# Kernel optimization log

Hardware: AMD Instinct MI355X
Metric: run time of the kernel (lower is better)

## Reference

```python
import jax, jax.numpy as jnp
import numpy as np

T, B, H, L2, C = 1132, 128, 13, 100, 10  # seq, batch, hidden, total layers (2x50), classes


def setup_inputs() -> dict:
    key = jax.random.key(0)
    ks = jax.random.split(key, 7)
    s = 1.0 / np.sqrt(H)  # torch LSTM/Linear default init scale
    return {
        "input": jax.random.normal(ks[0], (B, T, H), jnp.float32),
        "w_ih": jax.random.uniform(ks[1], (L2, 4 * H, H), jnp.float32, -s, s),
        "w_hh": jax.random.uniform(ks[2], (L2, 4 * H, H), jnp.float32, -s, s),
        "b_ih": jax.random.uniform(ks[3], (L2, 4 * H), jnp.float32, -s, s),
        "b_hh": jax.random.uniform(ks[4], (L2, 4 * H), jnp.float32, -s, s),
        "w_lin": jax.random.uniform(ks[5], (C, T * H), jnp.float32, -1.0 / np.sqrt(T * H), 1.0 / np.sqrt(T * H)),
        "b_lin": jax.random.uniform(ks[6], (C,), jnp.float32, -1.0 / np.sqrt(T * H), 1.0 / np.sqrt(T * H)),
    }


def _lstm_stack(x, w_ih, w_hh, b_ih, b_hh):
    # x: [T, B, H]; weights stacked over layers: [L, 4H, H], biases [L, 4H]
    def layer(x, params):
        Wih, Whh, bih, bhh = params
        # input contribution for all timesteps at once (one big GEMM)
        pre = jnp.einsum('tbf,gf->tbg', x, Wih) + bih + bhh  # [T, B, 4H]

        def step(carry, p):
            h, c = carry
            g = p + h @ Whh.T  # [B, 4H]
            i, f, gg, o = jnp.split(g, 4, axis=-1)  # torch gate order: i,f,g,o
            c = jax.nn.sigmoid(f) * c + jax.nn.sigmoid(i) * jnp.tanh(gg)
            h = jax.nn.sigmoid(o) * jnp.tanh(c)
            return (h, c), h

        h0 = jnp.zeros((x.shape[1], Whh.shape[1]), x.dtype)
        _, hs = jax.lax.scan(step, (h0, h0), pre)
        return hs, None

    x, _ = jax.lax.scan(layer, x, (w_ih, w_hh, b_ih, b_hh))
    return x


def reference(input, w_ih, w_hh, b_ih, b_hh, w_lin, b_lin):
    x = jnp.transpose(input, (1, 0, 2))  # [T, B, H] (time-major for scan)
    x = _lstm_stack(x, w_ih, w_hh, b_ih, b_hh)
    x = jnp.transpose(x, (1, 0, 2)).reshape(input.shape[0], -1)  # [B, T*H]
    logits = x @ w_lin.T + b_lin
    return jax.nn.softmax(logits, axis=1)
```

## Files before the change

kernel.cpp:

```cpp
#include <hip/hip_runtime.h>
#include <stdint.h>

#define T_SEQ  1132
#define BATCH  128
#define HID    13
#define G4     52
#define NLAYER 100
#define NPIPE  8
#define LPW    4
#define NWGP   25
#define NTHR   384
#define CH     4
#define NCH    283
#define RCL    4
#define RC     8
#define NCLS   10
#define FEAT   (T_SEQ*HID)
#define L2E    1.44269504f

#define CHUNK_U32 (CH*256)
#define FLAG_BYTES 65536
#define RING_U32_PER_WG ((size_t)RC * CHUNK_U32)
#define RING_BYTES ((size_t)(NPIPE*NWGP) * RING_U32_PER_WG * 4)

typedef float  f32x4 __attribute__((ext_vector_type(4)));
typedef __fp16 f16x4 __attribute__((ext_vector_type(4)));
typedef unsigned int u32x4 __attribute__((ext_vector_type(4)));
typedef unsigned long long u64x2 __attribute__((ext_vector_type(2)));

struct HL { f16x4 h; f16x4 l; };

__device__ __forceinline__ void f16split(float x, __fp16& hi, __fp16& lo) {
  hi = (__fp16)x;
  lo = (__fp16)(x - (float)hi);
}

__device__ __forceinline__ void lspin_ge(int* p, int need) {
  int v = __hip_atomic_load(p, __ATOMIC_ACQUIRE, __HIP_MEMORY_SCOPE_WORKGROUP);
  while (v < need) {
    __builtin_amdgcn_s_sleep(1);
    v = __hip_atomic_load(p, __ATOMIC_ACQUIRE, __HIP_MEMORY_SCOPE_WORKGROUP);
  }
}
__device__ __forceinline__ void gspin_ge(int* p, int need) {
  int v = __hip_atomic_load(p, __ATOMIC_RELAXED, __HIP_MEMORY_SCOPE_AGENT);
  while (v < need) {
    __builtin_amdgcn_s_sleep(1);
    v = __hip_atomic_load(p, __ATOMIC_RELAXED, __HIP_MEMORY_SCOPE_AGENT);
  }
}

__global__ __launch_bounds__(NTHR) void lstm_pipeline(
    const float* __restrict__ xin,
    const float* __restrict__ w_ih,
    const float* __restrict__ w_hh,
    const float* __restrict__ b_ih,
    const float* __restrict__ b_hh,
    int*      flags,
    uint32_t* ring,
    float*    act)
{
  const int wg   = blockIdx.x;
  const int pp   = wg / NWGP;
  const int wgi  = wg - pp * NWGP;
  const int tid  = threadIdx.x;
  const int lane = tid & 63;
  const int nt   = tid >> 6;
  const int quad = lane >> 4;
  const int b15  = lane & 15;
  const bool lastWG = (wgi == NWGP - 1);

  __shared__ __align__(16) uint32_t sXP[LPW][RCL][CH][256];
  __shared__ __align__(16) uint32_t sOutR[RCL][CH][256];
  __shared__ int sProg[LPW];
  __shared__ int sCons[LPW];
  __shared__ int sProgOut;
  __shared__ int sConsOut;

  int* flReadySelf = flags + ((pp * NWGP + wgi) * 2 + 0) * 16;
  int* flProgSelf  = flags + ((pp * NWGP + wgi) * 2 + 1) * 16;
  int* flReadyPrev = (wgi > 0) ? flags + ((pp * NWGP + wgi - 1) * 2 + 0) * 16 : flags;
  int* flProgNext  = (!lastWG) ? flags + ((pp * NWGP + wgi + 1) * 2 + 1) * 16 : flags;

  if (lane == 0) {
    if (nt == LPW + 1)
      __hip_atomic_store(flReadySelf, 0, __ATOMIC_RELAXED, __HIP_MEMORY_SCOPE_AGENT);
    if (nt == LPW)
      __hip_atomic_store(flProgSelf, 0, __ATOMIC_RELAXED, __HIP_MEMORY_SCOPE_AGENT);
  }
  if (tid < LPW) { sProg[tid] = 0; sCons[tid] = 0; }
  if (tid == 0) { sProgOut = 0; sConsOut = 0; }
  __syncthreads();

  if (nt < LPW) {
    const int l = wgi * LPW + nt;
    const bool lastL = (l == NLAYER - 1);

    f16x4 Axh[4], Axl[4], Ahh[4], Ahl[4];
    f32x4 biasv[4];
    #pragma unroll
    for (int mt = 0; mt < 4; ++mt) {
      const float gsc = (mt == 2) ? (2.0f * L2E) : (-L2E);
      #pragma unroll
      for (int jj = 0; jj < 4; ++jj) {
        int k = quad * 4 + jj;
        float wx = 0.f, wh = 0.f;
        if (b15 < HID && k < HID) {
          int g = mt * HID + b15;
          wx = w_ih[(size_t)(l * G4 + g) * HID + k];
          wh = w_hh[(size_t)(l * G4 + g) * HID + k];
        }
        wx *= gsc; wh *= gsc;
        __fp16 hi, lo;
        f16split(wx, hi, lo); Axh[mt][jj] = hi; Axl[mt][jj] = lo;
        f16split(wh, hi, lo); Ahh[mt][jj] = hi; Ahl[mt][jj] = lo;
      }
      #pragma unroll
      for (int r = 0; r < 4; ++r) {
        int jt = quad * 4 + r;
        biasv[mt][r] = (jt < HID)
            ? gsc * (b_ih[l * G4 + mt * HID + jt] + b_hh[l * G4 + mt * HID + jt]) : 0.f;
      }
    }

    f16x4 Bhh = (f16x4)0, Bhl = (f16x4)0;
    float cst[4] = {0.f, 0.f, 0.f, 0.f};

    #pragma unroll 1
    for (int ci = 0; ci < NCH; ++ci) {
      const int slot = ci & (RCL - 1);
      const int base = ci * CH;

      if (ci + 1 - RCL > 0) {
        if (nt < LPW - 1) lspin_ge(&sCons[nt + 1], ci + 1 - RCL);
        else              lspin_ge(&sConsOut,       ci + 1 - RCL);
      }

      lspin_ge(&sProg[nt], base + 1);
      f32x4 axc[4];
      {
        u32x4 bx = *(const u32x4*)&sXP[nt][slot][0][lane * 4];
        HL z = __builtin_bit_cast(HL, bx);
        #pragma unroll
        for (int mt = 0; mt < 4; ++mt) {
          f32x4 a = biasv[mt];
          a = __builtin_amdgcn_mfma_f32_16x16x16f16(Axh[mt], z.h, a, 0, 0, 0);
          a = __builtin_amdgcn_mfma_f32_16x16x16f16(Axl[mt], z.h, a, 0, 0, 0);
          a = __builtin_amdgcn_mfma_f32_16x16x16f16(Axh[mt], z.l, a, 0, 0, 0);
          axc[mt] = a;
        }
      }

      #pragma unroll
      for (int s = 0; s < CH; ++s) {
        f32x4 acc[4];
        #pragma unroll
        for (int mt = 0; mt < 4; ++mt) {
          f32x4 a = axc[mt];
          a = __builtin_amdgcn_mfma_f32_16x16x16f16(Ahh[mt], Bhh, a, 0, 0, 0);
          a = __builtin_amdgcn_mfma_f32_16x16x16f16(Ahl[mt], Bhh, a, 0, 0, 0);
          a = __builtin_amdgcn_mfma_f32_16x16x16f16(Ahh[mt], Bhl, a, 0, 0, 0);
          acc[mt] = a;
        }

        if (s < CH - 1) {
          lspin_ge(&sProg[nt], base + s + 2);
          u32x4 bx = *(const u32x4*)&sXP[nt][slot][s + 1][lane * 4];
          HL z = __builtin_bit_cast(HL, bx);
          #pragma unroll
          for (int mt = 0; mt < 4; ++mt) {
            f32x4 a = biasv[mt];
            a = __builtin_amdgcn_mfma_f32_16x16x16f16(Axh[mt], z.h, a, 0, 0, 0);
            a = __builtin_amdgcn_mfma_f32_16x16x16f16(Axl[mt], z.h, a, 0, 0, 0);
            a = __builtin_amdgcn_mfma_f32_16x16x16f16(Axh[mt], z.l, a, 0, 0, 0);
            axc[mt] = a;
          }
        }

        float hnv[4];
        #pragma unroll
        for (int r = 0; r < 4; ++r) {
          float eA = __builtin_amdgcn_exp2f(acc[0][r]);
          float eC = __builtin_amdgcn_exp2f(acc[1][r]);
          float eB = __builtin_amdgcn_exp2f(acc[2][r]);
          float eD = __builtin_amdgcn_exp2f(acc[3][r]);
          float ta = 1.0f + eA, tb = 1.0f + eB, tc = 1.0f + eC;
          float p  = ta * tb;
          float ri = __builtin_amdgcn_rcpf(p * tc);
          float num = fmaf((eB - 1.0f) * tc, 2.0f * L2E, cst[r] * p);
          float cn = num * ri;
          cst[r] = cn;
          float eE = __builtin_amdgcn_exp2f(fminf(cn, 100.0f));
          float r2 = __builtin_amdgcn_rcpf((eE + 1.0f) * (1.0f + eD));
          float h  = (eE - 1.0f) * r2;
          hnv[r] = h;
          __fp16 hi, lo; f16split(h, hi, lo);
          Bhh[r] = hi; Bhl[r] = lo;
        }
        if (nt < LPW - 1) {
          HL o; o.h = Bhh; o.l = Bhl;
          *(u32x4*)&sXP[nt + 1][slot][s][lane * 4] = __builtin_bit_cast(u32x4, o);
          if (lane == 0)
            __hip_atomic_store(&sProg[nt + 1], base + s + 1, __ATOMIC_RELEASE, __HIP_MEMORY_SCOPE_WORKGROUP);
        } else if (!lastL) {
          HL o; o.h = Bhh; o.l = Bhl;
          *(u32x4*)&sOutR[slot][s][lane * 4] = __builtin_bit_cast(u32x4, o);
          if (lane == 0)
            __hip_atomic_store(&sProgOut, base + s + 1, __ATOMIC_RELEASE, __HIP_MEMORY_SCOPE_WORKGROUP);
        } else {
          u32x4 w;
          #pragma unroll
          for (int r = 0; r < 4; ++r) w[r] = __float_as_uint(hnv[r]);
          *(u32x4*)&sOutR[slot][s][lane * 4] = w;
          if (lane == 0)
            __hip_atomic_store(&sProgOut, base + s + 1, __ATOMIC_RELEASE, __HIP_MEMORY_SCOPE_WORKGROUP);
        }
      }

      if (lane == 0)
        __hip_atomic_store(&sCons[nt], ci + 1, __ATOMIC_RELEASE, __HIP_MEMORY_SCOPE_WORKGROUP);
    }
  } else if (nt == LPW) {
    const uint32_t* ringprev = ring + (size_t)(pp * NWGP + wgi - 1) * RING_U32_PER_WG;
    const size_t    xrow     = (size_t)(pp * 16 + b15) * (T_SEQ * HID);

    #pragma unroll 1
    for (int cin = 0; cin < NCH; ++cin) {
      const int slot = cin & (RCL - 1);
      if (cin + 1 - RCL > 0) lspin_ge(&sCons[0], cin + 1 - RCL);

      if (wgi > 0) {
        gspin_ge(flReadyPrev, cin + 1);
        const uint64_t* src = (const uint64_t*)(ringprev + (size_t)(cin & (RC - 1)) * CHUNK_U32);
        uint64_t v[CH][2];
        #pragma unroll
        for (int s = 0; s < CH; ++s)
          #pragma unroll
          for (int w = 0; w < 2; ++w)
            v[s][w] = __hip_atomic_load(&src[s * 128 + lane * 2 + w],
                                        __ATOMIC_RELAXED, __HIP_MEMORY_SCOPE_AGENT);
        #pragma unroll
        for (int s = 0; s < CH; ++s) {
          u64x2 t = { v[s][0], v[s][1] };
          *(u32x4*)&sXP[0][slot][s][lane * 4] = __builtin_bit_cast(u32x4, t);
        }
        asm volatile("s_waitcnt vmcnt(0)" ::: "memory");
        if (lane == 0)
          __hip_atomic_store(flProgSelf, cin + 1, __ATOMIC_RELAXED, __HIP_MEMORY_SCOPE_AGENT);
      } else {
        const int t0 = cin * CH;
        #pragma unroll
        for (int s = 0; s < CH; ++s) {
          HL o;
          #pragma unroll
          for (int jj = 0; jj < 4; ++jj) {
            int k = quad * 4 + jj;
            float v = (k < HID) ? xin[xrow + (size_t)(t0 + s) * HID + k] : 0.f;
            __fp16 hi, lo; f16split(v, hi, lo);
            o.h[jj] = hi; o.l[jj] = lo;
          }
          *(u32x4*)&sXP[0][slot][s][lane * 4] = __builtin_bit_cast(u32x4, o);
        }
      }
      if (lane == 0)
        __hip_atomic_store(&sProg[0], (cin + 1) * CH, __ATOMIC_RELEASE, __HIP_MEMORY_SCOPE_WORKGROUP);
    }
  } else {
    uint32_t* ringmine = ring + (size_t)(pp * NWGP + wgi) * RING_U32_PER_WG;

    #pragma unroll 1
    for (int cout = 0; cout < NCH; ++cout) {
      const int slot = cout & (RCL - 1);
      lspin_ge(&sProgOut, (cout + 1) * CH);

      if (!lastWG) {
        if (cout + 1 - RC > 0) gspin_ge(flProgNext, cout + 1 - RC);
        uint64_t* dst = (uint64_t*)(ringmine + (size_t)(cout & (RC - 1)) * CHUNK_U32);
        #pragma unroll
        for (int s = 0; s < CH; ++s) {
          u32x4 v = *(const u32x4*)&sOutR[slot][s][lane * 4];
          u64x2 t = __builtin_bit_cast(u64x2, v);
          #pragma unroll
          for (int w = 0; w < 2; ++w)
            __hip_atomic_store(&dst[s * 128 + lane * 2 + w], t[w],
                               __ATOMIC_RELAXED, __HIP_MEMORY_SCOPE_AGENT);
        }
        asm volatile("s_waitcnt vmcnt(0)" ::: "memory");
        if (lane == 0) {
          __hip_atomic_store(flReadySelf, cout + 1, __ATOMIC_RELAXED, __HIP_MEMORY_SCOPE_AGENT);
          __hip_atomic_store(&sConsOut, cout + 1, __ATOMIC_RELEASE, __HIP_MEMORY_SCOPE_WORKGROUP);
        }
      } else {
        const int t0 = cout * CH;
        #pragma unroll
        for (int s = 0; s < CH; ++s) {
          u32x4 v = *(const u32x4*)&sOutR[slot][s][lane * 4];
          float* dst = act + (size_t)(t0 + s) * (BATCH * HID)
                     + (size_t)(pp * 16 + b15) * HID + quad * 4;
          #pragma unroll
          for (int r = 0; r < 4; ++r)
            if (quad * 4 + r < HID) dst[r] = __uint_as_float(v[r]);
        }
        if (lane == 0)
          __hip_atomic_store(&sConsOut, cout + 1, __ATOMIC_RELEASE, __HIP_MEMORY_SCOPE_WORKGROUP);
      }
    }
  }
}

__global__ __launch_bounds__(256) void linear_softmax(
    const float* __restrict__ act,
    const float* __restrict__ w_lin,
    const float* __restrict__ b_lin,
    float* __restrict__ out)
{
  const int b   = blockIdx.x;
  const int tid = threadIdx.x;
  float accv[NCLS];
  #pragma unroll
  for (int c = 0; c < NCLS; ++c) accv[c] = 0.f;

  for (int i = tid; i < FEAT; i += 256) {
    int t = i / HID; int jj = i - t * HID;
    float a = act[(size_t)t * (BATCH * HID) + b * HID + jj];
    #pragma unroll
    for (int c = 0; c < NCLS; ++c)
      accv[c] += a * w_lin[(size_t)c * FEAT + i];
  }

  __shared__ float red[NCLS][256];
  #pragma unroll
  for (int c = 0; c < NCLS; ++c) red[c][tid] = accv[c];
  __syncthreads();
  for (int off = 128; off > 0; off >>= 1) {
    if (tid < off) {
      #pragma unroll
      for (int c = 0; c < NCLS; ++c) red[c][tid] += red[c][tid + off];
    }
    __syncthreads();
  }
  if (tid == 0) {
    float lg[NCLS]; float mx = -1e30f;
    #pragma unroll
    for (int c = 0; c < NCLS; ++c) { lg[c] = red[c][0] + b_lin[c]; mx = fmaxf(mx, lg[c]); }
    float sum = 0.f;
    #pragma unroll
    for (int c = 0; c < NCLS; ++c) { lg[c] = __expf(lg[c] - mx); sum += lg[c]; }
    float inv = 1.0f / sum;
    #pragma unroll
    for (int c = 0; c < NCLS; ++c) out[b * NCLS + c] = lg[c] * inv;
  }
}

extern "C" void kernel_launch(void* const* d_in, const int* in_sizes, int n_in,
                              void* d_out, int out_size, void* d_ws, size_t ws_size,
                              hipStream_t stream) {
  const float* xin  = (const float*)d_in[0];
  const float* wih  = (const float*)d_in[1];
  const float* whh  = (const float*)d_in[2];
  const float* bih  = (const float*)d_in[3];
  const float* bhh  = (const float*)d_in[4];
  const float* wlin = (const float*)d_in[5];
  const float* blin = (const float*)d_in[6];

  char*     ws    = (char*)d_ws;
  int*      flags = (int*)ws;
  uint32_t* ring  = (uint32_t*)(ws + FLAG_BYTES);
  float*    act   = (float*)(ws + FLAG_BYTES + RING_BYTES);

  lstm_pipeline<<<NPIPE * NWGP, NTHR, 0, stream>>>(xin, wih, whh, bih, bhh, flags, ring, act);
  linear_softmax<<<BATCH, 256, 0, stream>>>(act, wlin, blin, (float*)d_out);
}
```

Before: 863.4 us.

## Add per-timestep granularity to inter-workgroup ring handoff when chunk not ready

The cross-workgroup ring producer and consumer warps previously waited for a full 4-timestep chunk before forwarding. Now, when a chunk is not yet complete, they forward each timestep as soon as it is available and publish progress per step, with the ready flag counting timesteps instead of chunks. This is meant to shorten the pipeline fill latency across the 25 chained workgroups in each pipe. The cost is more flag stores, more memory waits and more spin polling on the slow path.

```diff
diff --git a/kernel.cpp b/kernel.cpp
--- a/kernel.cpp
+++ b/kernel.cpp
@@ -227,28 +227,49 @@
     #pragma unroll 1
     for (int cin = 0; cin < NCH; ++cin) {
       const int slot = cin & (RCL - 1);
+      const int base = cin * CH;
       if (cin + 1 - RCL > 0) lspin_ge(&sCons[0], cin + 1 - RCL);
 
       if (wgi > 0) {
-        gspin_ge(flReadyPrev, cin + 1);
         const uint64_t* src = (const uint64_t*)(ringprev + (size_t)(cin & (RC - 1)) * CHUNK_U32);
-        uint64_t v[CH][2];
-        #pragma unroll
-        for (int s = 0; s < CH; ++s)
-          #pragma unroll
-          for (int w = 0; w < 2; ++w)
-            v[s][w] = __hip_atomic_load(&src[s * 128 + lane * 2 + w],
-                                        __ATOMIC_RELAXED, __HIP_MEMORY_SCOPE_AGENT);
-        #pragma unroll
-        for (int s = 0; s < CH; ++s) {
-          u64x2 t = { v[s][0], v[s][1] };
-          *(u32x4*)&sXP[0][slot][s][lane * 4] = __builtin_bit_cast(u32x4, t);
-        }
-        asm volatile("s_waitcnt vmcnt(0)" ::: "memory");
-        if (lane == 0)
-          __hip_atomic_store(flProgSelf, cin + 1, __ATOMIC_RELAXED, __HIP_MEMORY_SCOPE_AGENT);
+        int avail = __hip_atomic_load(flReadyPrev, __ATOMIC_RELAXED, __HIP_MEMORY_SCOPE_AGENT);
+        if (avail >= base + CH) {
+          uint64_t v[CH][2];
+          #pragma unroll
+          for (int s = 0; s < CH; ++s)
+            #pragma unroll
+            for (int w = 0; w < 2; ++w)
+              v[s][w] = __hip_atomic_load(&src[s * 128 + lane * 2 + w],
+                                          __ATOMIC_RELAXED, __HIP_MEMORY_SCOPE_AGENT);
+          #pragma unroll
+          for (int s = 0; s < CH; ++s) {
+            u64x2 t = { v[s][0], v[s][1] };
+            *(u32x4*)&sXP[0][slot][s][lane * 4] = __builtin_bit_cast(u32x4, t);
+          }
+          asm volatile("s_waitcnt vmcnt(0)" ::: "memory");
+          if (lane == 0) {
+            __hip_atomic_store(flProgSelf, cin + 1, __ATOMIC_RELAXED, __HIP_MEMORY_SCOPE_AGENT);
+            __hip_atomic_store(&sProg[0], base + CH, __ATOMIC_RELEASE, __HIP_MEMORY_SCOPE_WORKGROUP);
+          }
+        } else {
+          #pragma unroll
+          for (int s = 0; s < CH; ++s) {
+            gspin_ge(flReadyPrev, base + s + 1);
+            uint64_t v0 = __hip_atomic_load(&src[s * 128 + lane * 2 + 0],
+                                            __ATOMIC_RELAXED, __HIP_MEMORY_SCOPE_AGENT);
+            uint64_t v1 = __hip_atomic_load(&src[s * 128 + lane * 2 + 1],
+                                            __ATOMIC_RELAXED, __HIP_MEMORY_SCOPE_AGENT);
+            u64x2 t = { v0, v1 };
+            *(u32x4*)&sXP[0][slot][s][lane * 4] = __builtin_bit_cast(u32x4, t);
+            if (lane == 0)
+              __hip_atomic_store(&sProg[0], base + s + 1, __ATOMIC_RELEASE, __HIP_MEMORY_SCOPE_WORKGROUP);
+          }
+          asm volatile("s_waitcnt vmcnt(0)" ::: "memory");
+          if (lane == 0)
+            __hip_atomic_store(flProgSelf, cin + 1, __ATOMIC_RELAXED, __HIP_MEMORY_SCOPE_AGENT);
+        }
       } else {
-        const int t0 = cin * CH;
+        const int t0 = base;
         #pragma unroll
         for (int s = 0; s < CH; ++s) {
           HL o;
@@ -261,9 +282,9 @@
           }
           *(u32x4*)&sXP[0][slot][s][lane * 4] = __builtin_bit_cast(u32x4, o);
         }
-      }
-      if (lane == 0)
-        __hip_atomic_store(&sProg[0], (cin + 1) * CH, __ATOMIC_RELEASE, __HIP_MEMORY_SCOPE_WORKGROUP);
+        if (lane == 0)
+          __hip_atomic_store(&sProg[0], base + CH, __ATOMIC_RELEASE, __HIP_MEMORY_SCOPE_WORKGROUP);
+      }
     }
   } else {
     uint32_t* ringmine = ring + (size_t)(pp * NWGP + wgi) * RING_U32_PER_WG;
@@ -271,35 +292,55 @@
     #pragma unroll 1
     for (int cout = 0; cout < NCH; ++cout) {
       const int slot = cout & (RCL - 1);
-      lspin_ge(&sProgOut, (cout + 1) * CH);
+      const int base = cout * CH;
 
       if (!lastWG) {
         if (cout + 1 - RC > 0) gspin_ge(flProgNext, cout + 1 - RC);
         uint64_t* dst = (uint64_t*)(ringmine + (size_t)(cout & (RC - 1)) * CHUNK_U32);
+        int avail = __hip_atomic_load(&sProgOut, __ATOMIC_ACQUIRE, __HIP_MEMORY_SCOPE_WORKGROUP);
+        if (avail >= base + CH) {
+          #pragma unroll
+          for (int s = 0; s < CH; ++s) {
+            u32x4 v = *(const u32x4*)&sOutR[slot][s][lane * 4];
+            u64x2 t = __builtin_bit_cast(u64x2, v);
+            #pragma unroll
+            for (int w = 0; w < 2; ++w)
+              __hip_atomic_store(&dst[s * 128 + lane * 2 + w], t[w],
+                                 __ATOMIC_RELAXED, __HIP_MEMORY_SCOPE_AGENT);
+          }
+          asm volatile("s_waitcnt vmcnt(0)" ::: "memory");
+          if (lane == 0) {
+            __hip_atomic_store(flReadySelf, base + CH, __ATOMIC_RELAXED, __HIP_MEMORY_SCOPE_AGENT);
+            __hip_atomic_store(&sConsOut, cout + 1, __ATOMIC_RELEASE, __HIP_MEMORY_SCOPE_WORKGROUP);
+          }
+        } else {
+          #pragma unroll
+          for (int s = 0; s < CH; ++s) {
+            lspin_ge(&sProgOut, base + s + 1);
+            u32x4 v = *(const u32x4*)&sOutR[slot][s][lane * 4];
+            u64x2 t = __builtin_bit_cast(u64x2, v);
+            #pragma unroll
+            for (int w = 0; w < 2; ++w)
+              __hip_atomic_store(&dst[s * 128 + lane * 2 + w], t[w],
+                                 __ATOMIC_RELAXED, __HIP_MEMORY_SCOPE_AGENT);
+            asm volatile("s_waitcnt vmcnt(0)" ::: "memory");
+            if (lane == 0)
+              __hip_atomic_store(flReadySelf, base + s + 1, __ATOMIC_RELAXED, __HIP_MEMORY_SCOPE_AGENT);
+          }
+          if (lane == 0)
+            __hip_atomic_store(&sConsOut, cout + 1, __ATOMIC_RELEASE, __HIP_MEMORY_SCOPE_WORKGROUP);
+        }
+      } else {
+        lspin_ge(&sProgOut, base + CH);
+        const int t0 = base;
         #pragma unroll
         for (int s = 0; s < CH; ++s) {
           u32x4 v = *(const u32x4*)&sOutR[slot][s][lane * 4];
-          u64x2 t = __builtin_bit_cast(u64x2, v);
-          #pragma unroll
-          for (int w = 0; w < 2; ++w)
-            __hip_atomic_store(&dst[s * 128 + lane * 2 + w], t[w],
-                               __ATOMIC_RELAXED, __HIP_MEMORY_SCOPE_AGENT);
-        }
-        asm volatile("s_waitcnt vmcnt(0)" ::: "memory");
-        if (lane == 0) {
-          __hip_atomic_store(flReadySelf, cout + 1, __ATOMIC_RELAXED, __HIP_MEMORY_SCOPE_AGENT);
-          __hip_atomic_store(&sConsOut, cout + 1, __ATOMIC_RELEASE, __HIP_MEMORY_SCOPE_WORKGROUP);
-        }
-      } else {
-        const int t0 = cout * CH;
-        #pragma unroll
-        for (int s = 0; s < CH; ++s) {
-          u32x4 v = *(const u32x4*)&sOutR[slot][s][lane * 4];
-          float* dst = act + (size_t)(t0 + s) * (BATCH * HID)
-                     + (size_t)(pp * 16 + b15) * HID + quad * 4;
+          float* dstf = act + (size_t)(t0 + s) * (BATCH * HID)
+                      + (size_t)(pp * 16 + b15) * HID + quad * 4;
           #pragma unroll
           for (int r = 0; r < 4; ++r)
-            if (quad * 4 + r < HID) dst[r] = __uint_as_float(v[r]);
+            if (quad * 4 + r < HID) dstf[r] = __uint_as_float(v[r]);
         }
         if (lane == 0)
           __hip_atomic_store(&sConsOut, cout + 1, __ATOMIC_RELEASE, __HIP_MEMORY_SCOPE_WORKGROUP);
```

Result: slower. 883.1 us (+2.3%).

## Fuse linear+softmax head into last LSTM workgroup's output drain

Applied to the files above, without the earlier changes.

Instead of writing the final layer's hidden states to a global activation buffer and launching a separate linear+softmax kernel, the last workgroup of each pipeline accumulates the 10 class logits on the fly as chunks arrive, then reduces across the wavefront with shuffles and applies softmax. This removes the activation round-trip through global memory and the second kernel launch. The cost is extra FMA work and w_lin loads on the final drain wave, which could slow that stage if it sits on the critical path.

```diff
diff --git a/kernel.cpp b/kernel.cpp
--- a/kernel.cpp
+++ b/kernel.cpp
@@ -56,9 +56,11 @@
     const float* __restrict__ w_hh,
     const float* __restrict__ b_ih,
     const float* __restrict__ b_hh,
+    const float* __restrict__ w_lin,
+    const float* __restrict__ b_lin,
     int*      flags,
     uint32_t* ring,
-    float*    act)
+    float*    out)
 {
   const int wg   = blockIdx.x;
   const int pp   = wg / NWGP;
@@ -265,7 +267,7 @@
       if (lane == 0)
         __hip_atomic_store(&sProg[0], (cin + 1) * CH, __ATOMIC_RELEASE, __HIP_MEMORY_SCOPE_WORKGROUP);
     }
-  } else {
+  } else if (!lastWG) {
     uint32_t* ringmine = ring + (size_t)(pp * NWGP + wgi) * RING_U32_PER_WG;
 
     #pragma unroll 1
@@ -273,82 +275,76 @@
       const int slot = cout & (RCL - 1);
       lspin_ge(&sProgOut, (cout + 1) * CH);
 
-      if (!lastWG) {
-        if (cout + 1 - RC > 0) gspin_ge(flProgNext, cout + 1 - RC);
-        uint64_t* dst = (uint64_t*)(ringmine + (size_t)(cout & (RC - 1)) * CHUNK_U32);
-        #pragma unroll
-        for (int s = 0; s < CH; ++s) {
-          u32x4 v = *(const u32x4*)&sOutR[slot][s][lane * 4];
-          u64x2 t = __builtin_bit_cast(u64x2, v);
-          #pragma unroll
-          for (int w = 0; w < 2; ++w)
-            __hip_atomic_store(&dst[s * 128 + lane * 2 + w], t[w],
-                               __ATOMIC_RELAXED, __HIP_MEMORY_SCOPE_AGENT);
-        }
-        asm volatile("s_waitcnt vmcnt(0)" ::: "memory");
-        if (lane == 0) {
-          __hip_atomic_store(flReadySelf, cout + 1, __ATOMIC_RELAXED, __HIP_MEMORY_SCOPE_AGENT);
-          __hip_atomic_store(&sConsOut, cout + 1, __ATOMIC_RELEASE, __HIP_MEMORY_SCOPE_WORKGROUP);
-        }
-      } else {
-        const int t0 = cout * CH;
-        #pragma unroll
-        for (int s = 0; s < CH; ++s) {
-          u32x4 v = *(const u32x4*)&sOutR[slot][s][lane * 4];
-          float* dst = act + (size_t)(t0 + s) * (BATCH * HID)
-                     + (size_t)(pp * 16 + b15) * HID + quad * 4;
-          #pragma unroll
-          for (int r = 0; r < 4; ++r)
-            if (quad * 4 + r < HID) dst[r] = __uint_as_float(v[r]);
-        }
-        if (lane == 0)
-          __hip_atomic_store(&sConsOut, cout + 1, __ATOMIC_RELEASE, __HIP_MEMORY_SCOPE_WORKGROUP);
-      }
-    }
-  }
-}
-
-__global__ __launch_bounds__(256) void linear_softmax(
-    const float* __restrict__ act,
-    const float* __restrict__ w_lin,
-    const float* __restrict__ b_lin,
-    float* __restrict__ out)
-{
-  const int b   = blockIdx.x;
-  const int tid = threadIdx.x;
-  float accv[NCLS];
-  #pragma unroll
-  for (int c = 0; c < NCLS; ++c) accv[c] = 0.f;
-
-  for (int i = tid; i < FEAT; i += 256) {
-    int t = i / HID; int jj = i - t * HID;
-    float a = act[(size_t)t * (BATCH * HID) + b * HID + jj];
+      if (cout + 1 - RC > 0) gspin_ge(flProgNext, cout + 1 - RC);
+      uint64_t* dst = (uint64_t*)(ringmine + (size_t)(cout & (RC - 1)) * CHUNK_U32);
+      #pragma unroll
+      for (int s = 0; s < CH; ++s) {
+        u32x4 v = *(const u32x4*)&sOutR[slot][s][lane * 4];
+        u64x2 t = __builtin_bit_cast(u64x2, v);
+        #pragma unroll
+        for (int w = 0; w < 2; ++w)
+          __hip_atomic_store(&dst[s * 128 + lane * 2 + w], t[w],
+                             __ATOMIC_RELAXED, __HIP_MEMORY_SCOPE_AGENT);
+      }
+      asm volatile("s_waitcnt vmcnt(0)" ::: "memory");
+      if (lane == 0) {
+        __hip_atomic_store(flReadySelf, cout + 1, __ATOMIC_RELAXED, __HIP_MEMORY_SCOPE_AGENT);
+        __hip_atomic_store(&sConsOut, cout + 1, __ATOMIC_RELEASE, __HIP_MEMORY_SCOPE_WORKGROUP);
+      }
+    }
+  } else {
+    float accL[NCLS];
     #pragma unroll
-    for (int c = 0; c < NCLS; ++c)
-      accv[c] += a * w_lin[(size_t)c * FEAT + i];
-  }
-
-  __shared__ float red[NCLS][256];
-  #pragma unroll
-  for (int c = 0; c < NCLS; ++c) red[c][tid] = accv[c];
-  __syncthreads();
-  for (int off = 128; off > 0; off >>= 1) {
-    if (tid < off) {
-      #pragma unroll
-      for (int c = 0; c < NCLS; ++c) red[c][tid] += red[c][tid + off];
-    }
-    __syncthreads();
-  }
-  if (tid == 0) {
-    float lg[NCLS]; float mx = -1e30f;
+    for (int c = 0; c < NCLS; ++c) accL[c] = 0.f;
+    const int j0 = quad * 4;
+
+    #pragma unroll 1
+    for (int cout = 0; cout < NCH; ++cout) {
+      const int slot = cout & (RCL - 1);
+      lspin_ge(&sProgOut, (cout + 1) * CH);
+      const int t0 = cout * CH;
+
+      u32x4 v[CH];
+      #pragma unroll
+      for (int s = 0; s < CH; ++s)
+        v[s] = *(const u32x4*)&sOutR[slot][s][lane * 4];
+      if (lane == 0)
+        __hip_atomic_store(&sConsOut, cout + 1, __ATOMIC_RELEASE, __HIP_MEMORY_SCOPE_WORKGROUP);
+
+      #pragma unroll
+      for (int s = 0; s < CH; ++s) {
+        const int t = t0 + s;
+        #pragma unroll
+        for (int r = 0; r < 4; ++r) {
+          const int j = j0 + r;
+          if (j < HID) {
+            float h = __uint_as_float(v[s][r]);
+            const float* wl = w_lin + (size_t)t * HID + j;
+            #pragma unroll
+            for (int c = 0; c < NCLS; ++c)
+              accL[c] = fmaf(h, wl[(size_t)c * FEAT], accL[c]);
+          }
+        }
+      }
+    }
+
     #pragma unroll
-    for (int c = 0; c < NCLS; ++c) { lg[c] = red[c][0] + b_lin[c]; mx = fmaxf(mx, lg[c]); }
-    float sum = 0.f;
-    #pragma unroll
-    for (int c = 0; c < NCLS; ++c) { lg[c] = __expf(lg[c] - mx); sum += lg[c]; }
-    float inv = 1.0f / sum;
-    #pragma unroll
-    for (int c = 0; c < NCLS; ++c) out[b * NCLS + c] = lg[c] * inv;
+    for (int c = 0; c < NCLS; ++c) {
+      accL[c] += __shfl_xor(accL[c], 32);
+      accL[c] += __shfl_xor(accL[c], 16);
+    }
+    if (quad == 0) {
+      float lg[NCLS]; float mx = -1e30f;
+      #pragma unroll
+      for (int c = 0; c < NCLS; ++c) { lg[c] = accL[c] + b_lin[c]; mx = fmaxf(mx, lg[c]); }
+      float sum = 0.f;
+      #pragma unroll
+      for (int c = 0; c < NCLS; ++c) { lg[c] = __expf(lg[c] - mx); sum += lg[c]; }
+      float inv = 1.0f / sum;
+      #pragma unroll
+      for (int c = 0; c < NCLS; ++c)
+        out[(size_t)(pp * 16 + b15) * NCLS + c] = lg[c] * inv;
+    }
   }
 }
 
@@ -366,8 +362,8 @@
   char*     ws    = (char*)d_ws;
   int*      flags = (int*)ws;
   uint32_t* ring  = (uint32_t*)(ws + FLAG_BYTES);
-  float*    act   = (float*)(ws + FLAG_BYTES + RING_BYTES);
-
-  lstm_pipeline<<<NPIPE * NWGP, NTHR, 0, stream>>>(xin, wih, whh, bih, bhh, flags, ring, act);
-  linear_softmax<<<BATCH, 256, 0, stream>>>(act, wlin, blin, (float*)d_out);
-}
+
+  lstm_pipeline<<<NPIPE * NWGP, NTHR, 0, stream>>>(xin, wih, whh, bih, bhh,
+                                                   wlin, blin, flags, ring,
+                                                   (float*)d_out);
+}
```

Result: slower. 1.600 ms (+85.3%).
